# Kernel tuning notes

Measured on AMD Instinct MI355X. Metric: run time of the kernel, lower is better.

Reference implementation:

```python
import jax, jax.numpy as jnp
import numpy as np

EPS = 1e-5

def ln(x, w, b):
    mu = jnp.mean(x, axis=-1, keepdims=True)
    var = jnp.mean(jnp.square(x - mu), axis=-1, keepdims=True)
    return (x - mu) * jax.lax.rsqrt(var + EPS) * w + b

def setup_inputs() -> dict:
    key = jax.random.key(0)
    ks = jax.random.split(key, 4)
    B, H, W, C = 8, 224, 224, 96
    Cout = 2 * C  # 192
    x = jax.random.normal(ks[0], (B, H, W, C), dtype=jnp.float32)
    saliency_map = jax.random.uniform(ks[1], (B, H, W), dtype=jnp.float32)
    # PatchMerging reduction: Linear(4C -> 2C, bias=False), xavier_uniform init
    limit = float(np.sqrt(6.0 / (4 * C + Cout)))
    merge_w = jax.random.uniform(ks[2], (Cout, 4 * C), minval=-limit, maxval=limit, dtype=jnp.float32)
    return {
        "x": x,
        "saliency_map": saliency_map,
        "merge_w": merge_w,
        "merge_norm_w": jnp.ones((4 * C,), jnp.float32),
        "merge_norm_b": jnp.zeros((4 * C,), jnp.float32),
        "vss_norm_w": jnp.ones((Cout,), jnp.float32),
        "vss_norm_b": jnp.zeros((Cout,), jnp.float32),
        "asram_norm_w": jnp.ones((Cout,), jnp.float32),
        "asram_norm_b": jnp.zeros((Cout,), jnp.float32),
        "final_norm_w": jnp.ones((Cout,), jnp.float32),
        "final_norm_b": jnp.zeros((Cout,), jnp.float32),
    }

def reference(x, saliency_map, merge_w, merge_norm_w, merge_norm_b,
              vss_norm_w, vss_norm_b, asram_norm_w, asram_norm_b,
              final_norm_w, final_norm_b):
    # --- PatchMerging: [B,H,W,C] -> [B,H/2,W/2,2C] ---
    x0 = x[:, 0::2, 0::2, :]
    x1 = x[:, 1::2, 0::2, :]
    x2 = x[:, 0::2, 1::2, :]
    x3 = x[:, 1::2, 1::2, :]
    xm = jnp.concatenate([x0, x1, x2, x3], axis=-1)          # [B,H/2,W/2,4C]
    xm = ln(xm, merge_norm_w, merge_norm_b)
    xs = jnp.einsum('bhwi,oi->bhwo', xm, merge_w)            # [B,H/2,W/2,2C]
    # saliency adaptation (bilinear resize, align_corners=False); mock ASRAM ignores it
    B, Hn, Wn, _ = xs.shape
    _sal = jax.image.resize(saliency_map[:, None], (B, 1, Hn, Wn), method='bilinear')
    del _sal  # unused by mock ASRAM, kept for fidelity of the dataflow
    # --- Mock DualVSSBlock: x + LayerNorm(x) ---
    xv = xs + ln(xs, vss_norm_w, vss_norm_b)
    # --- Mock ASRAM: LayerNorm over channels (permute round-trip is a no-op here) ---
    xa = ln(xv, asram_norm_w, asram_norm_b)
    # --- Final LayerNorm ---
    return ln(xa, final_norm_w, final_norm_b)
```

## Files before the change

### kernel.cpp

```cpp
#include <hip/hip_runtime.h>
#include <hip/hip_bf16.h>
#include <cstdint>
#include <cstddef>

typedef float f32x4  __attribute__((ext_vector_type(4)));
typedef short bf16x8 __attribute__((ext_vector_type(8)));
typedef int   i32x4  __attribute__((ext_vector_type(4)));

#define LN_EPS 1e-5f

static __device__ __forceinline__ unsigned short f2bf(float f) {
    __hip_bfloat16 h = __float2bfloat16(f);
    union { __hip_bfloat16 b; unsigned short u; } cv; cv.b = h;
    return cv.u;
}
static __device__ __forceinline__ float bf2f(unsigned short h) {
    return __uint_as_float(((unsigned int)h) << 16);
}

__global__ void prep_w_kernel(const float* __restrict__ W,
                              const float* __restrict__ g,
                              unsigned short* __restrict__ wsh) {
    int o = blockIdx.x * 256 + threadIdx.x;
    if (o >= 192 * 384) return;
    int j    = o & 7;
    int lane = (o >> 3) & 63;
    int t    = o >> 9;
    int nf   = t % 12;
    int kk   = t / 12;
    int n = nf * 16 + (lane & 15);
    int k = kk * 32 + (lane >> 4) * 8 + j;
    wsh[o] = f2bf(g[k] * W[n * 384 + k]);
}

__global__ void prep_sc_kernel(const float* __restrict__ W,
                               const float* __restrict__ g,
                               const float* __restrict__ b,
                               float* __restrict__ s2,
                               float* __restrict__ c0) {
    const int o = blockIdx.x;
    const int j = threadIdx.x;
    const float* wr = W + o * 384;
    float a = 0.f, c = 0.f;
    #pragma unroll
    for (int i = 0; i < 6; i++) {
        const int k = j + 64 * i;
        float w = wr[k];
        a += g[k] * w; c += b[k] * w;
    }
    #pragma unroll
    for (int d = 1; d < 64; d <<= 1) { a += __shfl_xor(a, d); c += __shfl_xor(c, d); }
    if (j == 0) { s2[o] = a; c0[o] = c; }
}

__global__ __launch_bounds__(256, 3)
void fused_split(const float* __restrict__ x,
                 const unsigned short* __restrict__ wsh,
                 const float* __restrict__ s2p, const float* __restrict__ c0p,
                 const float* __restrict__ vw, const float* __restrict__ vb,
                 const float* __restrict__ aw, const float* __restrict__ ab,
                 const float* __restrict__ fw, const float* __restrict__ fb,
                 float* __restrict__ out) {
    __shared__ __align__(16) unsigned char lds[25088];

    const int tid = threadIdx.x;
    const int r   = tid >> 3;
    const int u   = tid & 7;
    const int q   = u >> 1;
    const int hh  = u & 1;

    const int wv = tid >> 6;
    const int l  = tid & 63;
    const int g  = l >> 4;
    const int cl = l & 15;

    float mu, rs;
    i32x4 PH[6], PL[6];

    {
        const int R   = blockIdx.x * 32 + r;
        const int b   = R / 12544;
        const int rem = R - b * 12544;
        const int h2  = rem / 112;
        const int w2  = rem - h2 * 112;
        const int h   = 2 * h2 + (q & 1);
        const int w   = 2 * w2 + (q >> 1);
        const f32x4* src = (const f32x4*)(x + (((size_t)b * 224 + h) * 224 + w) * 96 + hh * 48);
        f32x4 v[12];
        #pragma unroll
        for (int i = 0; i < 12; i++) v[i] = src[i];

        #pragma unroll
        for (int p = 0; p < 6; p++) {
            union { unsigned short u16[8]; i32x4 v4; } ph, pl;
            #pragma unroll
            for (int half = 0; half < 2; half++) {
                const int i = 2 * p + half;
                #pragma unroll
                for (int e = 0; e < 4; e++) {
                    float a = v[i][e];
                    unsigned short hi = f2bf(a);
                    ph.u16[4 * half + e] = hi;
                    pl.u16[4 * half + e] = f2bf(a - bf2f(hi));
                }
            }
            PH[p] = ph.v4; PL[p] = pl.v4;
        }
        if (u < 4) {
            #pragma unroll
            for (int p = 0; p < 6; p++) {
                const int sl   = 6 * u + p;
                const int boff = (sl * 16) ^ ((r & 7) << 4);
                *(i32x4*)(&lds[r * 384 + boff])         = PH[p];
                *(i32x4*)(&lds[12288 + r * 384 + boff]) = PL[p];
            }
        }
        float s = 0.f;
        #pragma unroll
        for (int i = 0; i < 12; i++) {
            #pragma unroll
            for (int e = 0; e < 4; e++) s += v[i][e];
        }
        s += __shfl_xor(s, 1); s += __shfl_xor(s, 2); s += __shfl_xor(s, 4);
        mu = s * (1.f / 384.f);
        float sd = 0.f;
        #pragma unroll
        for (int i = 0; i < 12; i++) {
            #pragma unroll
            for (int e = 0; e < 4; e++) { float d = v[i][e] - mu; sd += d * d; }
        }
        sd += __shfl_xor(sd, 1); sd += __shfl_xor(sd, 2); sd += __shfl_xor(sd, 4);
        rs = rsqrtf(sd * (1.f / 384.f) + LN_EPS);
    }

    f32x4 acc[2][3];
    #pragma unroll
    for (int mf = 0; mf < 2; mf++)
        #pragma unroll
        for (int t = 0; t < 3; t++) acc[mf][t] = (f32x4){0.f, 0.f, 0.f, 0.f};

    bf16x8 B0[3], B1[3], B2[3];
    auto issue = [&](int KK, bf16x8* Bb) {
        const bf16x8* bp = (const bf16x8*)wsh + ((KK * 12 + 3 * wv) * 64 + l);
        asm volatile("global_load_dwordx4 %0, %1, off" : "=v"(Bb[0]) : "v"(bp));
        asm volatile("global_load_dwordx4 %0, %1, off" : "=v"(Bb[1]) : "v"(bp + 64));
        asm volatile("global_load_dwordx4 %0, %1, off" : "=v"(Bb[2]) : "v"(bp + 128));
    };
    auto consume = [&](int KK, const bf16x8* Bb) {
        const int kl = KK >= 6 ? KK - 6 : KK;
        #pragma unroll
        for (int mf = 0; mf < 2; mf++) {
            const int row  = 16 * mf + cl;
            const int boff = (kl * 64 + g * 16) ^ ((row & 7) << 4);
            bf16x8 afh = *(const bf16x8*)(&lds[row * 384 + boff]);
            bf16x8 afl = *(const bf16x8*)(&lds[12288 + row * 384 + boff]);
            #pragma unroll
            for (int t = 0; t < 3; t++) {
                acc[mf][t] = __builtin_amdgcn_mfma_f32_16x16x32_bf16(afh, Bb[t], acc[mf][t], 0, 0, 0);
                acc[mf][t] = __builtin_amdgcn_mfma_f32_16x16x32_bf16(afl, Bb[t], acc[mf][t], 0, 0, 0);
            }
        }
    };

    issue(0, B0); issue(1, B1);
    __syncthreads();

    #define STEP(KK, BUF, NXTBUF, VM)                                   \
        do {                                                            \
            if ((KK) + 2 < 12) issue((KK) + 2, NXTBUF);                 \
            asm volatile("s_waitcnt vmcnt(" #VM ")" ::: "memory");      \
            __builtin_amdgcn_sched_barrier(0);                          \
            consume((KK), BUF);                                         \
        } while (0)

    STEP(0, B0, B2, 6);
    STEP(1, B1, B0, 6);
    STEP(2, B2, B1, 6);
    STEP(3, B0, B2, 6);
    STEP(4, B1, B0, 6);
    STEP(5, B2, B1, 6);

    __syncthreads();
    if (u >= 4) {
        #pragma unroll
        for (int p = 0; p < 6; p++) {
            const int sl   = 6 * (u - 4) + p;
            const int boff = (sl * 16) ^ ((r & 7) << 4);
            *(i32x4*)(&lds[r * 384 + boff])         = PH[p];
            *(i32x4*)(&lds[12288 + r * 384 + boff]) = PL[p];
        }
    }
    __syncthreads();

    STEP(6,  B0, B2, 6);
    STEP(7,  B1, B0, 6);
    STEP(8,  B2, B1, 6);
    STEP(9,  B0, B2, 6);
    STEP(10, B1, B0, 3);
    STEP(11, B2, B1, 0);
    #undef STEP
    __builtin_amdgcn_sched_barrier(0);
    __syncthreads();

    {
        float* xsl = (float*)lds;
        #pragma unroll
        for (int mf = 0; mf < 2; mf++)
            #pragma unroll
            for (int t = 0; t < 3; t++) {
                const int col = 48 * wv + 16 * t + cl;
                #pragma unroll
                for (int rg = 0; rg < 4; rg++) {
                    const int row = 16 * mf + 4 * g + rg;
                    xsl[row * 196 + col] = acc[mf][t][rg];
                }
            }
    }
    __syncthreads();

    {
        const float* rowp = (const float*)lds + r * 196 + u * 24;
        float vv[24];
        #pragma unroll
        for (int i = 0; i < 6; i++) {
            f32x4 t4 = *(const f32x4*)(rowp + 4 * i);
            #pragma unroll
            for (int e = 0; e < 4; e++) vv[4 * i + e] = t4[e];
        }
        {
            const f32x4* s2v = (const f32x4*)(s2p + u * 24);
            const f32x4* c0v = (const f32x4*)(c0p + u * 24);
            #pragma unroll
            for (int i = 0; i < 6; i++) {
                f32x4 sv = s2v[i], cv = c0v[i];
                #pragma unroll
                for (int e = 0; e < 4; e++)
                    vv[4 * i + e] = rs * (vv[4 * i + e] - mu * sv[e]) + cv[e];
            }
        }
        float s1 = 0.f;
        #pragma unroll
        for (int i = 0; i < 24; i++) s1 += vv[i];
        s1 += __shfl_xor(s1, 1); s1 += __shfl_xor(s1, 2); s1 += __shfl_xor(s1, 4);
        const float mu1 = s1 * (1.f / 192.f);
        float d1 = 0.f;
        #pragma unroll
        for (int i = 0; i < 24; i++) { float d = vv[i] - mu1; d1 += d * d; }
        d1 += __shfl_xor(d1, 1); d1 += __shfl_xor(d1, 2); d1 += __shfl_xor(d1, 4);
        const float r1 = rsqrtf(d1 * (1.f / 192.f) + LN_EPS);

        const f32x4* vwv = (const f32x4*)(vw + u * 24);
        const f32x4* vbv = (const f32x4*)(vb + u * 24);
        float s2s = 0.f;
        #pragma unroll
        for (int i = 0; i < 6; i++) {
            f32x4 w4 = vwv[i], b4 = vbv[i];
            #pragma unroll
            for (int e = 0; e < 4; e++) {
                float xs0 = vv[4 * i + e];
                float xv0 = xs0 + (xs0 - mu1) * r1 * w4[e] + b4[e];
                vv[4 * i + e] = xv0;
                s2s += xv0;
            }
        }
        s2s += __shfl_xor(s2s, 1); s2s += __shfl_xor(s2s, 2); s2s += __shfl_xor(s2s, 4);
        const float mu2 = s2s * (1.f / 192.f);
        float d2 = 0.f;
        #pragma unroll
        for (int i = 0; i < 24; i++) { float d = vv[i] - mu2; d2 += d * d; }
        d2 += __shfl_xor(d2, 1); d2 += __shfl_xor(d2, 2); d2 += __shfl_xor(d2, 4);
        const float r2 = rsqrtf(d2 * (1.f / 192.f) + LN_EPS);

        const f32x4* awv = (const f32x4*)(aw + u * 24);
        const f32x4* abv = (const f32x4*)(ab + u * 24);
        float s3 = 0.f;
        #pragma unroll
        for (int i = 0; i < 6; i++) {
            f32x4 w4 = awv[i], b4 = abv[i];
            #pragma unroll
            for (int e = 0; e < 4; e++) {
                float xa0 = (vv[4 * i + e] - mu2) * r2 * w4[e] + b4[e];
                vv[4 * i + e] = xa0;
                s3 += xa0;
            }
        }
        s3 += __shfl_xor(s3, 1); s3 += __shfl_xor(s3, 2); s3 += __shfl_xor(s3, 4);
        const float mu3 = s3 * (1.f / 192.f);
        float d3 = 0.f;
        #pragma unroll
        for (int i = 0; i < 24; i++) { float d = vv[i] - mu3; d3 += d * d; }
        d3 += __shfl_xor(d3, 1); d3 += __shfl_xor(d3, 2); d3 += __shfl_xor(d3, 4);
        const float r3 = rsqrtf(d3 * (1.f / 192.f) + LN_EPS);

        const f32x4* fwv = (const f32x4*)(fw + u * 24);
        const f32x4* fbv = (const f32x4*)(fb + u * 24);
        float* op = out + (size_t)(blockIdx.x * 32 + r) * 192 + u * 24;
        #pragma unroll
        for (int i = 0; i < 6; i++) {
            f32x4 w4 = fwv[i], b4 = fbv[i];
            f32x4 o4;
            #pragma unroll
            for (int e = 0; e < 4; e++)
                o4[e] = (vv[4 * i + e] - mu3) * r3 * w4[e] + b4[e];
            *(f32x4*)(op + 4 * i) = o4;
        }
    }
}

__global__ __launch_bounds__(256, 3)
void fused_fallback(const float* __restrict__ x,
                    const float* __restrict__ Wf,
                    const float* __restrict__ mw, const float* __restrict__ mb,
                    const float* __restrict__ vw, const float* __restrict__ vb,
                    const float* __restrict__ aw, const float* __restrict__ ab,
                    const float* __restrict__ fw, const float* __restrict__ fb,
                    float* __restrict__ out) {
    __shared__ __align__(16) unsigned char lds[49152];
    const int tid = threadIdx.x;
    const int r   = tid >> 3;
    const int u   = tid & 7;
    const int q   = u >> 1;
    const int hh  = u & 1;
    const int wv = tid >> 6;
    const int l  = tid & 63;
    const int g  = l >> 4;
    const int cl = l & 15;

    {
        const int R   = blockIdx.x * 32 + r;
        const int b   = R / 12544;
        const int rem = R - b * 12544;
        const int h2  = rem / 112;
        const int w2  = rem - h2 * 112;
        const int h   = 2 * h2 + (q & 1);
        const int w   = 2 * w2 + (q >> 1);
        const f32x4* src = (const f32x4*)(x + (((size_t)b * 224 + h) * 224 + w) * 96 + hh * 48);
        f32x4 v[12];
        #pragma unroll
        for (int i = 0; i < 12; i++) v[i] = src[i];
        float s = 0.f;
        #pragma unroll
        for (int i = 0; i < 12; i++)
            #pragma unroll
            for (int e = 0; e < 4; e++) s += v[i][e];
        s += __shfl_xor(s, 1); s += __shfl_xor(s, 2); s += __shfl_xor(s, 4);
        const float mu = s * (1.f / 384.f);
        float sd = 0.f;
        #pragma unroll
        for (int i = 0; i < 12; i++)
            #pragma unroll
            for (int e = 0; e < 4; e++) { float d = v[i][e] - mu; sd += d * d; }
        sd += __shfl_xor(sd, 1); sd += __shfl_xor(sd, 2); sd += __shfl_xor(sd, 4);
        const float rs = rsqrtf(sd * (1.f / 384.f) + LN_EPS);
        const f32x4* mwv = (const f32x4*)(mw + q * 96 + hh * 48);
        const f32x4* mbv = (const f32x4*)(mb + q * 96 + hh * 48);
        #pragma unroll
        for (int p = 0; p < 6; p++) {
            union { unsigned short u16[8]; i32x4 v4; } ph, pl;
            #pragma unroll
            for (int half = 0; half < 2; half++) {
                const int i = 2 * p + half;
                f32x4 w4 = mwv[i], b4 = mbv[i];
                #pragma unroll
                for (int e = 0; e < 4; e++) {
                    float a = (v[i][e] - mu) * rs * w4[e] + b4[e];
                    unsigned short hi = f2bf(a);
                    ph.u16[4 * half + e] = hi;
                    pl.u16[4 * half + e] = f2bf(a - bf2f(hi));
                }
            }
            const int slot = 6 * u + p;
            const int boff = (slot * 16) ^ ((r & 7) << 4);
            *(i32x4*)(&lds[r * 768 + boff])         = ph.v4;
            *(i32x4*)(&lds[24576 + r * 768 + boff]) = pl.v4;
        }
    }
    __syncthreads();

    f32x4 acc[2][3];
    #pragma unroll
    for (int mf = 0; mf < 2; mf++)
        #pragma unroll
        for (int t = 0; t < 3; t++) acc[mf][t] = (f32x4){0.f, 0.f, 0.f, 0.f};
    #pragma unroll
    for (int kk = 0; kk < 12; kk++) {
        bf16x8 bh[3];
        #pragma unroll
        for (int t = 0; t < 3; t++) {
            const int n = (3 * wv + t) * 16 + cl;
            const float* wp = Wf + n * 384 + kk * 32 + g * 8;
            f32x4 lo = *(const f32x4*)wp;
            f32x4 hi4 = *(const f32x4*)(wp + 4);
            bf16x8 hbb;
            #pragma unroll
            for (int e = 0; e < 4; e++) { hbb[e] = (short)f2bf(lo[e]); hbb[4 + e] = (short)f2bf(hi4[e]); }
            bh[t] = hbb;
        }
        #pragma unroll
        for (int mf = 0; mf < 2; mf++) {
            const int row  = 16 * mf + cl;
            const int boff = (kk * 64 + g * 16) ^ ((row & 7) << 4);
            bf16x8 afh = *(const bf16x8*)(&lds[row * 768 + boff]);
            bf16x8 afl = *(const bf16x8*)(&lds[24576 + row * 768 + boff]);
            #pragma unroll
            for (int t = 0; t < 3; t++) {
                acc[mf][t] = __builtin_amdgcn_mfma_f32_16x16x32_bf16(afh, bh[t], acc[mf][t], 0, 0, 0);
                acc[mf][t] = __builtin_amdgcn_mfma_f32_16x16x32_bf16(afl, bh[t], acc[mf][t], 0, 0, 0);
            }
        }
    }
    __syncthreads();
    {
        float* xsl = (float*)lds;
        #pragma unroll
        for (int mf = 0; mf < 2; mf++)
            #pragma unroll
            for (int t = 0; t < 3; t++) {
                const int col = 48 * wv + 16 * t + cl;
                #pragma unroll
                for (int rg = 0; rg < 4; rg++) {
                    const int row = 16 * mf + 4 * g + rg;
                    xsl[row * 196 + col] = acc[mf][t][rg];
                }
            }
    }
    __syncthreads();
    {
        const float* rowp = (const float*)lds + r * 196 + u * 24;
        float vv[24];
        #pragma unroll
        for (int i = 0; i < 6; i++) {
            f32x4 t4 = *(const f32x4*)(rowp + 4 * i);
            #pragma unroll
            for (int e = 0; e < 4; e++) vv[4 * i + e] = t4[e];
        }
        float s1 = 0.f;
        #pragma unroll
        for (int i = 0; i < 24; i++) s1 += vv[i];
        s1 += __shfl_xor(s1, 1); s1 += __shfl_xor(s1, 2); s1 += __shfl_xor(s1, 4);
        const float mu1 = s1 * (1.f / 192.f);
        float d1 = 0.f;
        #pragma unroll
        for (int i = 0; i < 24; i++) { float d = vv[i] - mu1; d1 += d * d; }
        d1 += __shfl_xor(d1, 1); d1 += __shfl_xor(d1, 2); d1 += __shfl_xor(d1, 4);
        const float r1 = rsqrtf(d1 * (1.f / 192.f) + LN_EPS);
        const f32x4* vwv = (const f32x4*)(vw + u * 24);
        const f32x4* vbv = (const f32x4*)(vb + u * 24);
        float s2s = 0.f;
        #pragma unroll
        for (int i = 0; i < 6; i++) {
            f32x4 w4 = vwv[i], b4 = vbv[i];
            #pragma unroll
            for (int e = 0; e < 4; e++) {
                float xs0 = vv[4 * i + e];
                float xv0 = xs0 + (xs0 - mu1) * r1 * w4[e] + b4[e];
                vv[4 * i + e] = xv0;
                s2s += xv0;
            }
        }
        s2s += __shfl_xor(s2s, 1); s2s += __shfl_xor(s2s, 2); s2s += __shfl_xor(s2s, 4);
        const float mu2 = s2s * (1.f / 192.f);
        float d2 = 0.f;
        #pragma unroll
        for (int i = 0; i < 24; i++) { float d = vv[i] - mu2; d2 += d * d; }
        d2 += __shfl_xor(d2, 1); d2 += __shfl_xor(d2, 2); d2 += __shfl_xor(d2, 4);
        const float r2 = rsqrtf(d2 * (1.f / 192.f) + LN_EPS);
        const f32x4* awv = (const f32x4*)(aw + u * 24);
        const f32x4* abv = (const f32x4*)(ab + u * 24);
        float s3 = 0.f;
        #pragma unroll
        for (int i = 0; i < 6; i++) {
            f32x4 w4 = awv[i], b4 = abv[i];
            #pragma unroll
            for (int e = 0; e < 4; e++) {
                float xa0 = (vv[4 * i + e] - mu2) * r2 * w4[e] + b4[e];
                vv[4 * i + e] = xa0;
                s3 += xa0;
            }
        }
        s3 += __shfl_xor(s3, 1); s3 += __shfl_xor(s3, 2); s3 += __shfl_xor(s3, 4);
        const float mu3 = s3 * (1.f / 192.f);
        float d3 = 0.f;
        #pragma unroll
        for (int i = 0; i < 24; i++) { float d = vv[i] - mu3; d3 += d * d; }
        d3 += __shfl_xor(d3, 1); d3 += __shfl_xor(d3, 2); d3 += __shfl_xor(d3, 4);
        const float r3 = rsqrtf(d3 * (1.f / 192.f) + LN_EPS);
        const f32x4* fwv = (const f32x4*)(fw + u * 24);
        const f32x4* fbv = (const f32x4*)(fb + u * 24);
        float* op = out + (size_t)(blockIdx.x * 32 + r) * 192 + u * 24;
        #pragma unroll
        for (int i = 0; i < 6; i++) {
            f32x4 w4 = fwv[i], b4 = fbv[i];
            f32x4 o4;
            #pragma unroll
            for (int e = 0; e < 4; e++)
                o4[e] = (vv[4 * i + e] - mu3) * r3 * w4[e] + b4[e];
            *(f32x4*)(op + 4 * i) = o4;
        }
    }
}

extern "C" void kernel_launch(void* const* d_in, const int* in_sizes, int n_in,
                              void* d_out, int out_size, void* d_ws, size_t ws_size,
                              hipStream_t stream) {
    const float* x  = (const float*)d_in[0];
    const float* W  = (const float*)d_in[2];
    const float* mw = (const float*)d_in[3];
    const float* mb = (const float*)d_in[4];
    const float* vw = (const float*)d_in[5];
    const float* vb = (const float*)d_in[6];
    const float* aw = (const float*)d_in[7];
    const float* ab = (const float*)d_in[8];
    const float* fw = (const float*)d_in[9];
    const float* fb = (const float*)d_in[10];
    float* out = (float*)d_out;

    const int rows   = 8 * 112 * 112;
    const int blocks = rows / 32;

    unsigned short* wsh = (unsigned short*)d_ws;
    float* s2 = (float*)((char*)d_ws + 192 * 384 * 2);
    float* c0 = s2 + 192;

    if (ws_size >= (size_t)(192 * 384 * 2 + 2 * 192 * 4)) {
        prep_w_kernel<<<288, 256, 0, stream>>>(W, mw, wsh);
        prep_sc_kernel<<<192, 64, 0, stream>>>(W, mw, mb, s2, c0);
        fused_split<<<blocks, 256, 0, stream>>>(x, wsh, s2, c0,
                                                vw, vb, aw, ab, fw, fb, out);
    } else {
        fused_fallback<<<blocks, 256, 0, stream>>>(x, W, mw, mb, vw, vb,
                                                   aw, ab, fw, fb, out);
    }
}
```

Before: 79.59 us.

## Drop manual triple-buffered weight prefetch and raise occupancy target to six blocks

Replaces the hand-scheduled inline-asm triple-buffered B-fragment prefetch pipeline with plain compiler-scheduled loads inside two unrolled K loops. It also raises the launch-bounds minimum blocks per CU from 3 to 6, which caps registers per thread. The aim is to hide global-load latency through more resident waves instead of explicit prefetch. The risks are register spills under the tighter cap and exposed load latency if the compiler does not hoist the loads. LDS use of about 25KB per block also limits how many blocks can actually be resident.

```diff
diff --git a/kernel.cpp b/kernel.cpp
--- a/kernel.cpp
+++ b/kernel.cpp
@@ -53,7 +53,7 @@
     if (j == 0) { s2[o] = a; c0[o] = c; }
 }
 
-__global__ __launch_bounds__(256, 3)
+__global__ __launch_bounds__(256, 6)
 void fused_split(const float* __restrict__ x,
                  const unsigned short* __restrict__ wsh,
                  const float* __restrict__ s2p, const float* __restrict__ c0p,
@@ -132,6 +132,7 @@
         sd += __shfl_xor(sd, 1); sd += __shfl_xor(sd, 2); sd += __shfl_xor(sd, 4);
         rs = rsqrtf(sd * (1.f / 384.f) + LN_EPS);
     }
+    __syncthreads();
 
     f32x4 acc[2][3];
     #pragma unroll
@@ -139,15 +140,43 @@
         #pragma unroll
         for (int t = 0; t < 3; t++) acc[mf][t] = (f32x4){0.f, 0.f, 0.f, 0.f};
 
-    bf16x8 B0[3], B1[3], B2[3];
-    auto issue = [&](int KK, bf16x8* Bb) {
-        const bf16x8* bp = (const bf16x8*)wsh + ((KK * 12 + 3 * wv) * 64 + l);
-        asm volatile("global_load_dwordx4 %0, %1, off" : "=v"(Bb[0]) : "v"(bp));
-        asm volatile("global_load_dwordx4 %0, %1, off" : "=v"(Bb[1]) : "v"(bp + 64));
-        asm volatile("global_load_dwordx4 %0, %1, off" : "=v"(Bb[2]) : "v"(bp + 128));
-    };
-    auto consume = [&](int KK, const bf16x8* Bb) {
-        const int kl = KK >= 6 ? KK - 6 : KK;
+    #pragma unroll
+    for (int kk = 0; kk < 6; kk++) {
+        bf16x8 bh[3];
+        const bf16x8* bph = (const bf16x8*)wsh + ((kk * 12 + 3 * wv) * 64 + l);
+        bh[0] = bph[0]; bh[1] = bph[64]; bh[2] = bph[128];
+        #pragma unroll
+        for (int mf = 0; mf < 2; mf++) {
+            const int row  = 16 * mf + cl;
+            const int boff = (kk * 64 + g * 16) ^ ((row & 7) << 4);
+            bf16x8 afh = *(const bf16x8*)(&lds[row * 384 + boff]);
+            bf16x8 afl = *(const bf16x8*)(&lds[12288 + row * 384 + boff]);
+            #pragma unroll
+            for (int t = 0; t < 3; t++) {
+                acc[mf][t] = __builtin_amdgcn_mfma_f32_16x16x32_bf16(afh, bh[t], acc[mf][t], 0, 0, 0);
+                acc[mf][t] = __builtin_amdgcn_mfma_f32_16x16x32_bf16(afl, bh[t], acc[mf][t], 0, 0, 0);
+            }
+        }
+    }
+
+    __syncthreads();
+    if (u >= 4) {
+        #pragma unroll
+        for (int p = 0; p < 6; p++) {
+            const int sl   = 6 * (u - 4) + p;
+            const int boff = (sl * 16) ^ ((r & 7) << 4);
+            *(i32x4*)(&lds[r * 384 + boff])         = PH[p];
+            *(i32x4*)(&lds[12288 + r * 384 + boff]) = PL[p];
+        }
+    }
+    __syncthreads();
+
+    #pragma unroll
+    for (int kk = 6; kk < 12; kk++) {
+        bf16x8 bh[3];
+        const bf16x8* bph = (const bf16x8*)wsh + ((kk * 12 + 3 * wv) * 64 + l);
+        bh[0] = bph[0]; bh[1] = bph[64]; bh[2] = bph[128];
+        const int kl = kk - 6;
         #pragma unroll
         for (int mf = 0; mf < 2; mf++) {
             const int row  = 16 * mf + cl;
@@ -156,50 +185,11 @@
             bf16x8 afl = *(const bf16x8*)(&lds[12288 + row * 384 + boff]);
             #pragma unroll
             for (int t = 0; t < 3; t++) {
-                acc[mf][t] = __builtin_amdgcn_mfma_f32_16x16x32_bf16(afh, Bb[t], acc[mf][t], 0, 0, 0);
-                acc[mf][t] = __builtin_amdgcn_mfma_f32_16x16x32_bf16(afl, Bb[t], acc[mf][t], 0, 0, 0);
-            }
-        }
-    };
-
-    issue(0, B0); issue(1, B1);
-    __syncthreads();
-
-    #define STEP(KK, BUF, NXTBUF, VM)                                   \
-        do {                                                            \
-            if ((KK) + 2 < 12) issue((KK) + 2, NXTBUF);                 \
-            asm volatile("s_waitcnt vmcnt(" #VM ")" ::: "memory");      \
-            __builtin_amdgcn_sched_barrier(0);                          \
-            consume((KK), BUF);                                         \
-        } while (0)
-
-    STEP(0, B0, B2, 6);
-    STEP(1, B1, B0, 6);
-    STEP(2, B2, B1, 6);
-    STEP(3, B0, B2, 6);
-    STEP(4, B1, B0, 6);
-    STEP(5, B2, B1, 6);
-
-    __syncthreads();
-    if (u >= 4) {
-        #pragma unroll
-        for (int p = 0; p < 6; p++) {
-            const int sl   = 6 * (u - 4) + p;
-            const int boff = (sl * 16) ^ ((r & 7) << 4);
-            *(i32x4*)(&lds[r * 384 + boff])         = PH[p];
-            *(i32x4*)(&lds[12288 + r * 384 + boff]) = PL[p];
-        }
-    }
-    __syncthreads();
-
-    STEP(6,  B0, B2, 6);
-    STEP(7,  B1, B0, 6);
-    STEP(8,  B2, B1, 6);
-    STEP(9,  B0, B2, 6);
-    STEP(10, B1, B0, 3);
-    STEP(11, B2, B1, 0);
-    #undef STEP
-    __builtin_amdgcn_sched_barrier(0);
+                acc[mf][t] = __builtin_amdgcn_mfma_f32_16x16x32_bf16(afh, bh[t], acc[mf][t], 0, 0, 0);
+                acc[mf][t] = __builtin_amdgcn_mfma_f32_16x16x32_bf16(afl, bh[t], acc[mf][t], 0, 0, 0);
+            }
+        }
+    }
     __syncthreads();
 
     {
```

Result: slower. 146.8 us (+84.4%).
